# Optimization experiments

Hardware: AMD Instinct MI355X
Metric: run time of the kernel (lower is better)

Reference implementation:

```python
import jax, jax.numpy as jnp
import numpy as np

B, T, D, H = 8, 128, 768, 768  # batch, num tokens (actual==virtual), dim, hidden_dim
LN_EPS = 1e-5


def setup_inputs() -> dict:
    key = jax.random.key(0)
    ks = jax.random.split(key, 7)
    s1 = 1.0 / np.sqrt(D)  # torch nn.Linear init scale (uniform bound)
    s2 = 1.0 / np.sqrt(H)
    return {
        "x": jax.random.normal(ks[0], (B, T, D), dtype=jnp.float32),
        "gamma": jnp.ones((T, D), dtype=jnp.float32),
        "beta": jnp.zeros((T, D), dtype=jnp.float32),
        "W1": jax.random.uniform(ks[1], (T, D, H), minval=-s1, maxval=s1, dtype=jnp.float32),
        "b1": jax.random.uniform(ks[2], (T, H), minval=-s1, maxval=s1, dtype=jnp.float32),
        "W2": jax.random.uniform(ks[3], (T, H, D), minval=-s2, maxval=s2, dtype=jnp.float32),
        "b2": jax.random.uniform(ks[4], (T, D), minval=-s2, maxval=s2, dtype=jnp.float32),
    }


def reference(x, gamma, beta, W1, b1, W2, b2):
    # Per-token FeedForward with distinct weights per token position, fully batched
    # (equivalent to the per-token Python loop in the torch module, with
    # num_actual_tokens == num_virtual_tokens so no repeat happens).
    mu = jnp.mean(x, axis=-1, keepdims=True)
    var = jnp.mean(jnp.square(x - mu), axis=-1, keepdims=True)
    xn = (x - mu) * jax.lax.rsqrt(var + LN_EPS)
    xn = xn * gamma[None] + beta[None]                      # [B,T,D]
    h = jnp.einsum('btd,tdh->bth', xn, W1) + b1[None]       # [B,T,H]
    h = jax.nn.gelu(h, approximate=False)                   # torch nn.GELU default (erf)
    out = jnp.einsum('bth,thd->btd', h, W2) + b2[None]      # [B,T,D]
    return out + x  # residual
```

## Files before the change

### kernel.cpp

```cpp
#include <hip/hip_runtime.h>
#include <math.h>

#define TB 8
#define TT 128
#define TD 768
#define TH 768
#define LN_EPS 1e-5f

__global__ __launch_bounds__(256) void ln_kernel(
    const float* __restrict__ x,
    const float* __restrict__ gamma,
    const float* __restrict__ beta,
    float* __restrict__ xn) {
  const int w = threadIdx.x >> 6, lane = threadIdx.x & 63;
  const int r = blockIdx.x * 4 + w;
  const int t = r & (TT - 1);
  const int b = r >> 7;
  const float* xr = x + (size_t)r * TD;

  float v[12];
  float s = 0.f, ss = 0.f;
#pragma unroll
  for (int i = 0; i < 3; ++i) {
    float4 f = *(const float4*)(xr + i * 256 + lane * 4);
    v[i * 4 + 0] = f.x; v[i * 4 + 1] = f.y;
    v[i * 4 + 2] = f.z; v[i * 4 + 3] = f.w;
    s += f.x + f.y + f.z + f.w;
    ss += f.x * f.x + f.y * f.y + f.z * f.z + f.w * f.w;
  }
#pragma unroll
  for (int off = 32; off; off >>= 1) {
    s  += __shfl_down(s, off, 64);
    ss += __shfl_down(ss, off, 64);
  }
  s = __shfl(s, 0, 64); ss = __shfl(ss, 0, 64);
  const float mu   = s * (1.f / TD);
  const float var  = ss * (1.f / TD) - mu * mu;
  const float rstd = rsqrtf(var + LN_EPS);

#pragma unroll
  for (int i = 0; i < 3; ++i) {
    const int d = i * 256 + lane * 4;
    float4 g  = *(const float4*)(gamma + (size_t)t * TD + d);
    float4 be = *(const float4*)(beta  + (size_t)t * TD + d);
    float* o = xn + ((size_t)t * TD + d) * TB + b;
    o[0 * TB] = (v[i * 4 + 0] - mu) * rstd * g.x + be.x;
    o[1 * TB] = (v[i * 4 + 1] - mu) * rstd * g.y + be.y;
    o[2 * TB] = (v[i * 4 + 2] - mu) * rstd * g.z + be.z;
    o[3 * TB] = (v[i * 4 + 3] - mu) * rstd * g.w + be.w;
  }
}

__global__ __launch_bounds__(256) void ff1_kernel(
    const float* __restrict__ xn,
    const float* __restrict__ W1,
    const float* __restrict__ b1,
    float* __restrict__ hbuf) {
  __shared__ float st[TD * TB];
  __shared__ float red[4][8][128];
  const int tid = threadIdx.x;
  const int w = tid >> 6, lane = tid & 63;
  const int t = blockIdx.x / 6, slice = blockIdx.x % 6;

  {
    const float4* src = (const float4*)(xn + (size_t)t * TD * TB);
    float4* dst = (float4*)st;
#pragma unroll
    for (int i = 0; i < 6; ++i) dst[tid + i * 256] = src[tid + i * 256];
  }
  __syncthreads();

  const int half = lane >> 5;
  const int cg = (lane & 31) * 4;
  const int c = slice * 128 + cg;
  const int r0 = w * 192 + half * 96;
  const float* wp = W1 + ((size_t)t * TD + r0) * TH + c;
  const float* xb = st + r0 * TB;

  float acc[8][4];
#pragma unroll
  for (int b = 0; b < 8; ++b)
#pragma unroll
    for (int j = 0; j < 4; ++j) acc[b][j] = 0.f;

#pragma unroll 4
  for (int d = 0; d < 96; ++d) {
    const float4 wv = *(const float4*)wp;
    wp += TH;
    const float4 xa = *(const float4*)(xb + d * 8);
    const float4 xc = *(const float4*)(xb + d * 8 + 4);
    const float xv[8] = {xa.x, xa.y, xa.z, xa.w, xc.x, xc.y, xc.z, xc.w};
#pragma unroll
    for (int b = 0; b < 8; ++b) {
      acc[b][0] = fmaf(xv[b], wv.x, acc[b][0]);
      acc[b][1] = fmaf(xv[b], wv.y, acc[b][1]);
      acc[b][2] = fmaf(xv[b], wv.z, acc[b][2]);
      acc[b][3] = fmaf(xv[b], wv.w, acc[b][3]);
    }
  }

#pragma unroll
  for (int b = 0; b < 8; ++b)
#pragma unroll
    for (int j = 0; j < 4; ++j)
      acc[b][j] += __shfl_xor(acc[b][j], 32, 64);

  if (lane < 32) {
#pragma unroll
    for (int b = 0; b < 8; ++b)
      *(float4*)&red[w][b][cg] =
          make_float4(acc[b][0], acc[b][1], acc[b][2], acc[b][3]);
  }
  __syncthreads();

  {
    const int col = tid >> 1;
    const int bq = (tid & 1) * 4;
    const int cc = slice * 128 + col;
    const float bias = b1[(size_t)t * TH + cc];
    float4 o;
    float* po = (float*)&o;
#pragma unroll
    for (int i = 0; i < 4; ++i) {
      float v = red[0][bq + i][col] + red[1][bq + i][col] +
                red[2][bq + i][col] + red[3][bq + i][col] + bias;
      po[i] = 0.5f * v * (1.f + erff(v * 0.7071067811865476f));
    }
    *(float4*)(hbuf + ((size_t)t * TH + cc) * TB + bq) = o;
  }
}

__global__ __launch_bounds__(256) void ff2_kernel(
    const float* __restrict__ hbuf,
    const float* __restrict__ W2,
    const float* __restrict__ b2,
    const float* __restrict__ x,
    float* __restrict__ out) {
  __shared__ float st[TH * TB];
  __shared__ float red[4][8][128];
  const int tid = threadIdx.x;
  const int w = tid >> 6, lane = tid & 63;
  const int t = blockIdx.x / 6, slice = blockIdx.x % 6;

  {
    const float4* src = (const float4*)(hbuf + (size_t)t * TH * TB);
    float4* dst = (float4*)st;
#pragma unroll
    for (int i = 0; i < 6; ++i) dst[tid + i * 256] = src[tid + i * 256];
  }
  __syncthreads();

  const int half = lane >> 5;
  const int cg = (lane & 31) * 4;
  const int c = slice * 128 + cg;
  const int r0 = w * 192 + half * 96;
  const float* wp = W2 + ((size_t)t * TH + r0) * TD + c;
  const float* hb = st + r0 * TB;

  float acc[8][4];
#pragma unroll
  for (int b = 0; b < 8; ++b)
#pragma unroll
    for (int j = 0; j < 4; ++j) acc[b][j] = 0.f;

#pragma unroll 4
  for (int d = 0; d < 96; ++d) {
    const float4 wv = *(const float4*)wp;
    wp += TD;
    const float4 ha = *(const float4*)(hb + d * 8);
    const float4 hc = *(const float4*)(hb + d * 8 + 4);
    const float hv[8] = {ha.x, ha.y, ha.z, ha.w, hc.x, hc.y, hc.z, hc.w};
#pragma unroll
    for (int b = 0; b < 8; ++b) {
      acc[b][0] = fmaf(hv[b], wv.x, acc[b][0]);
      acc[b][1] = fmaf(hv[b], wv.y, acc[b][1]);
      acc[b][2] = fmaf(hv[b], wv.z, acc[b][2]);
      acc[b][3] = fmaf(hv[b], wv.w, acc[b][3]);
    }
  }

#pragma unroll
  for (int b = 0; b < 8; ++b)
#pragma unroll
    for (int j = 0; j < 4; ++j)
      acc[b][j] += __shfl_xor(acc[b][j], 32, 64);

  if (lane < 32) {
#pragma unroll
    for (int b = 0; b < 8; ++b)
      *(float4*)&red[w][b][cg] =
          make_float4(acc[b][0], acc[b][1], acc[b][2], acc[b][3]);
  }
  __syncthreads();

  {
    const int col = tid >> 1;
    const int bq = (tid & 1) * 4;
    const int cc = slice * 128 + col;
    const float bias = b2[(size_t)t * TD + cc];
#pragma unroll
    for (int i = 0; i < 4; ++i) {
      const size_t off = ((size_t)(bq + i) * TT + t) * TD + cc;
      float v = red[0][bq + i][col] + red[1][bq + i][col] +
                red[2][bq + i][col] + red[3][bq + i][col] + bias + x[off];
      out[off] = v;
    }
  }
}

extern "C" void kernel_launch(void* const* d_in, const int* in_sizes, int n_in,
                              void* d_out, int out_size, void* d_ws, size_t ws_size,
                              hipStream_t stream) {
  const float* x     = (const float*)d_in[0];
  const float* gamma = (const float*)d_in[1];
  const float* beta  = (const float*)d_in[2];
  const float* W1    = (const float*)d_in[3];
  const float* b1    = (const float*)d_in[4];
  const float* W2    = (const float*)d_in[5];
  const float* b2    = (const float*)d_in[6];
  float* out = (float*)d_out;

  float* xn   = (float*)d_ws;
  float* hbuf = xn + (size_t)TT * TD * TB;

  ln_kernel<<<256, 256, 0, stream>>>(x, gamma, beta, xn);
  ff1_kernel<<<TT * 6, 256, 0, stream>>>(xn, W1, b1, hbuf);
  ff2_kernel<<<TT * 6, 256, 0, stream>>>(hbuf, W2, b2, x, out);
}
```

Baseline: 121.3 us.

## Fuse LayerNorm into first GEMM and switch activations to batch-major layout

Folds the LayerNorm kernel into ff1, so each block normalizes its token's 8 batch rows straight into shared memory. This removes one launch and the xn workspace round trip. Shared and intermediate buffers change from d-major interleaved to [batch][dim] layout, which gives vectorized float4 stores for hbuf and the output and coalesced residual reads. The inner loops now load 4 weight rows per step and float4 activations per batch. The catch is that LayerNorm is recomputed in all 6 slice blocks per token (6x redundant LN work and x reads), and the stride-768 shared reads may cause bank conflicts.

```diff
diff --git a/kernel.cpp b/kernel.cpp
--- a/kernel.cpp
+++ b/kernel.cpp
@@ -7,75 +7,58 @@
 #define TH 768
 #define LN_EPS 1e-5f
 
-__global__ __launch_bounds__(256) void ln_kernel(
+__global__ __launch_bounds__(256) void ff1_kernel(
     const float* __restrict__ x,
     const float* __restrict__ gamma,
     const float* __restrict__ beta,
-    float* __restrict__ xn) {
-  const int w = threadIdx.x >> 6, lane = threadIdx.x & 63;
-  const int r = blockIdx.x * 4 + w;
-  const int t = r & (TT - 1);
-  const int b = r >> 7;
-  const float* xr = x + (size_t)r * TD;
-
-  float v[12];
-  float s = 0.f, ss = 0.f;
-#pragma unroll
-  for (int i = 0; i < 3; ++i) {
-    float4 f = *(const float4*)(xr + i * 256 + lane * 4);
-    v[i * 4 + 0] = f.x; v[i * 4 + 1] = f.y;
-    v[i * 4 + 2] = f.z; v[i * 4 + 3] = f.w;
-    s += f.x + f.y + f.z + f.w;
-    ss += f.x * f.x + f.y * f.y + f.z * f.z + f.w * f.w;
-  }
-#pragma unroll
-  for (int off = 32; off; off >>= 1) {
-    s  += __shfl_down(s, off, 64);
-    ss += __shfl_down(ss, off, 64);
-  }
-  s = __shfl(s, 0, 64); ss = __shfl(ss, 0, 64);
-  const float mu   = s * (1.f / TD);
-  const float var  = ss * (1.f / TD) - mu * mu;
-  const float rstd = rsqrtf(var + LN_EPS);
-
-#pragma unroll
-  for (int i = 0; i < 3; ++i) {
-    const int d = i * 256 + lane * 4;
-    float4 g  = *(const float4*)(gamma + (size_t)t * TD + d);
-    float4 be = *(const float4*)(beta  + (size_t)t * TD + d);
-    float* o = xn + ((size_t)t * TD + d) * TB + b;
-    o[0 * TB] = (v[i * 4 + 0] - mu) * rstd * g.x + be.x;
-    o[1 * TB] = (v[i * 4 + 1] - mu) * rstd * g.y + be.y;
-    o[2 * TB] = (v[i * 4 + 2] - mu) * rstd * g.z + be.z;
-    o[3 * TB] = (v[i * 4 + 3] - mu) * rstd * g.w + be.w;
-  }
-}
-
-__global__ __launch_bounds__(256) void ff1_kernel(
-    const float* __restrict__ xn,
     const float* __restrict__ W1,
     const float* __restrict__ b1,
     float* __restrict__ hbuf) {
-  __shared__ float st[TD * TB];
+  __shared__ float st[TB][TD];
   __shared__ float red[4][8][128];
   const int tid = threadIdx.x;
   const int w = tid >> 6, lane = tid & 63;
+  const int half = lane >> 5, l32 = lane & 31;
   const int t = blockIdx.x / 6, slice = blockIdx.x % 6;
 
   {
-    const float4* src = (const float4*)(xn + (size_t)t * TD * TB);
-    float4* dst = (float4*)st;
-#pragma unroll
-    for (int i = 0; i < 6; ++i) dst[tid + i * 256] = src[tid + i * 256];
-  }
-  __syncthreads();
-
-  const int half = lane >> 5;
-  const int cg = (lane & 31) * 4;
+    const int b = w * 2 + half;
+    const float* xr = x + ((size_t)b * TT + t) * TD;
+    float4 v[6];
+    float s = 0.f, ss = 0.f;
+#pragma unroll
+    for (int i = 0; i < 6; ++i) {
+      v[i] = *(const float4*)(xr + i * 128 + l32 * 4);
+      s += v[i].x + v[i].y + v[i].z + v[i].w;
+      ss += v[i].x * v[i].x + v[i].y * v[i].y + v[i].z * v[i].z + v[i].w * v[i].w;
+    }
+#pragma unroll
+    for (int off = 16; off; off >>= 1) {
+      s  += __shfl_xor(s, off, 64);
+      ss += __shfl_xor(ss, off, 64);
+    }
+    const float mu   = s * (1.f / TD);
+    const float var  = ss * (1.f / TD) - mu * mu;
+    const float rstd = rsqrtf(var + LN_EPS);
+#pragma unroll
+    for (int i = 0; i < 6; ++i) {
+      const int d = i * 128 + l32 * 4;
+      const float4 g  = *(const float4*)(gamma + (size_t)t * TD + d);
+      const float4 be = *(const float4*)(beta  + (size_t)t * TD + d);
+      float4 o;
+      o.x = (v[i].x - mu) * rstd * g.x + be.x;
+      o.y = (v[i].y - mu) * rstd * g.y + be.y;
+      o.z = (v[i].z - mu) * rstd * g.z + be.z;
+      o.w = (v[i].w - mu) * rstd * g.w + be.w;
+      *(float4*)&st[b][d] = o;
+    }
+  }
+  __syncthreads();
+
+  const int cg = l32 * 4;
   const int c = slice * 128 + cg;
   const int r0 = w * 192 + half * 96;
   const float* wp = W1 + ((size_t)t * TD + r0) * TH + c;
-  const float* xb = st + r0 * TB;
 
   float acc[8][4];
 #pragma unroll
@@ -83,20 +66,25 @@
 #pragma unroll
     for (int j = 0; j < 4; ++j) acc[b][j] = 0.f;
 
-#pragma unroll 4
-  for (int d = 0; d < 96; ++d) {
-    const float4 wv = *(const float4*)wp;
-    wp += TH;
-    const float4 xa = *(const float4*)(xb + d * 8);
-    const float4 xc = *(const float4*)(xb + d * 8 + 4);
-    const float xv[8] = {xa.x, xa.y, xa.z, xa.w, xc.x, xc.y, xc.z, xc.w};
-#pragma unroll
-    for (int b = 0; b < 8; ++b) {
-      acc[b][0] = fmaf(xv[b], wv.x, acc[b][0]);
-      acc[b][1] = fmaf(xv[b], wv.y, acc[b][1]);
-      acc[b][2] = fmaf(xv[b], wv.z, acc[b][2]);
-      acc[b][3] = fmaf(xv[b], wv.w, acc[b][3]);
-    }
+#pragma unroll 2
+  for (int dd = 0; dd < 96; dd += 4) {
+    float4 wv[4];
+#pragma unroll
+    for (int k = 0; k < 4; ++k) wv[k] = *(const float4*)(wp + k * TH);
+    wp += 4 * TH;
+    float4 xq[8];
+#pragma unroll
+    for (int b = 0; b < 8; ++b) xq[b] = *(const float4*)&st[b][r0 + dd];
+#pragma unroll
+    for (int k = 0; k < 4; ++k)
+#pragma unroll
+      for (int b = 0; b < 8; ++b) {
+        const float xv = ((const float*)&xq[b])[k];
+        acc[b][0] = fmaf(xv, wv[k].x, acc[b][0]);
+        acc[b][1] = fmaf(xv, wv[k].y, acc[b][1]);
+        acc[b][2] = fmaf(xv, wv[k].z, acc[b][2]);
+        acc[b][3] = fmaf(xv, wv[k].w, acc[b][3]);
+      }
   }
 
 #pragma unroll
@@ -114,19 +102,20 @@
   __syncthreads();
 
   {
-    const int col = tid >> 1;
-    const int bq = (tid & 1) * 4;
-    const int cc = slice * 128 + col;
-    const float bias = b1[(size_t)t * TH + cc];
+    const int b = tid >> 5;
+    const int colq = (tid & 31) * 4;
+    const int cc = slice * 128 + colq;
+    const float4 bias = *(const float4*)(b1 + (size_t)t * TH + cc);
     float4 o;
     float* po = (float*)&o;
-#pragma unroll
-    for (int i = 0; i < 4; ++i) {
-      float v = red[0][bq + i][col] + red[1][bq + i][col] +
-                red[2][bq + i][col] + red[3][bq + i][col] + bias;
-      po[i] = 0.5f * v * (1.f + erff(v * 0.7071067811865476f));
-    }
-    *(float4*)(hbuf + ((size_t)t * TH + cc) * TB + bq) = o;
+    const float* pb = (const float*)&bias;
+#pragma unroll
+    for (int k = 0; k < 4; ++k) {
+      float vv = red[0][b][colq + k] + red[1][b][colq + k] +
+                 red[2][b][colq + k] + red[3][b][colq + k] + pb[k];
+      po[k] = 0.5f * vv * (1.f + erff(vv * 0.7071067811865476f));
+    }
+    *(float4*)(hbuf + ((size_t)t * TB + b) * TH + cc) = o;
   }
 }
 
@@ -136,26 +125,25 @@
     const float* __restrict__ b2,
     const float* __restrict__ x,
     float* __restrict__ out) {
-  __shared__ float st[TH * TB];
+  __shared__ float st[TB][TH];
   __shared__ float red[4][8][128];
   const int tid = threadIdx.x;
   const int w = tid >> 6, lane = tid & 63;
+  const int half = lane >> 5, l32 = lane & 31;
   const int t = blockIdx.x / 6, slice = blockIdx.x % 6;
 
   {
-    const float4* src = (const float4*)(hbuf + (size_t)t * TH * TB);
-    float4* dst = (float4*)st;
+    const float4* src = (const float4*)(hbuf + (size_t)t * TB * TH);
+    float4* dst = (float4*)&st[0][0];
 #pragma unroll
     for (int i = 0; i < 6; ++i) dst[tid + i * 256] = src[tid + i * 256];
   }
   __syncthreads();
 
-  const int half = lane >> 5;
-  const int cg = (lane & 31) * 4;
+  const int cg = l32 * 4;
   const int c = slice * 128 + cg;
   const int r0 = w * 192 + half * 96;
   const float* wp = W2 + ((size_t)t * TH + r0) * TD + c;
-  const float* hb = st + r0 * TB;
 
   float acc[8][4];
 #pragma unroll
@@ -163,20 +151,25 @@
 #pragma unroll
     for (int j = 0; j < 4; ++j) acc[b][j] = 0.f;
 
-#pragma unroll 4
-  for (int d = 0; d < 96; ++d) {
-    const float4 wv = *(const float4*)wp;
-    wp += TD;
-    const float4 ha = *(const float4*)(hb + d * 8);
-    const float4 hc = *(const float4*)(hb + d * 8 + 4);
-    const float hv[8] = {ha.x, ha.y, ha.z, ha.w, hc.x, hc.y, hc.z, hc.w};
-#pragma unroll
-    for (int b = 0; b < 8; ++b) {
-      acc[b][0] = fmaf(hv[b], wv.x, acc[b][0]);
-      acc[b][1] = fmaf(hv[b], wv.y, acc[b][1]);
-      acc[b][2] = fmaf(hv[b], wv.z, acc[b][2]);
-      acc[b][3] = fmaf(hv[b], wv.w, acc[b][3]);
-    }
+#pragma unroll 2
+  for (int dd = 0; dd < 96; dd += 4) {
+    float4 wv[4];
+#pragma unroll
+    for (int k = 0; k < 4; ++k) wv[k] = *(const float4*)(wp + k * TD);
+    wp += 4 * TD;
+    float4 hq[8];
+#pragma unroll
+    for (int b = 0; b < 8; ++b) hq[b] = *(const float4*)&st[b][r0 + dd];
+#pragma unroll
+    for (int k = 0; k < 4; ++k)
+#pragma unroll
+      for (int b = 0; b < 8; ++b) {
+        const float hv = ((const float*)&hq[b])[k];
+        acc[b][0] = fmaf(hv, wv[k].x, acc[b][0]);
+        acc[b][1] = fmaf(hv, wv[k].y, acc[b][1]);
+        acc[b][2] = fmaf(hv, wv[k].z, acc[b][2]);
+        acc[b][3] = fmaf(hv, wv[k].w, acc[b][3]);
+      }
   }
 
 #pragma unroll
@@ -194,17 +187,21 @@
   __syncthreads();
 
   {
-    const int col = tid >> 1;
-    const int bq = (tid & 1) * 4;
-    const int cc = slice * 128 + col;
-    const float bias = b2[(size_t)t * TD + cc];
-#pragma unroll
-    for (int i = 0; i < 4; ++i) {
-      const size_t off = ((size_t)(bq + i) * TT + t) * TD + cc;
-      float v = red[0][bq + i][col] + red[1][bq + i][col] +
-                red[2][bq + i][col] + red[3][bq + i][col] + bias + x[off];
-      out[off] = v;
-    }
+    const int b = tid >> 5;
+    const int colq = (tid & 31) * 4;
+    const int cc = slice * 128 + colq;
+    const size_t off = ((size_t)b * TT + t) * TD + cc;
+    const float4 bias = *(const float4*)(b2 + (size_t)t * TD + cc);
+    const float4 xres = *(const float4*)(x + off);
+    float4 o;
+    float* po = (float*)&o;
+    const float* pb = (const float*)&bias;
+    const float* px = (const float*)&xres;
+#pragma unroll
+    for (int k = 0; k < 4; ++k)
+      po[k] = red[0][b][colq + k] + red[1][b][colq + k] +
+              red[2][b][colq + k] + red[3][b][colq + k] + pb[k] + px[k];
+    *(float4*)(out + off) = o;
   }
 }
 
@@ -220,10 +217,8 @@
   const float* b2    = (const float*)d_in[6];
   float* out = (float*)d_out;
 
-  float* xn   = (float*)d_ws;
-  float* hbuf = xn + (size_t)TT * TD * TB;
-
-  ln_kernel<<<256, 256, 0, stream>>>(x, gamma, beta, xn);
-  ff1_kernel<<<TT * 6, 256, 0, stream>>>(xn, W1, b1, hbuf);
+  float* hbuf = (float*)d_ws;
+
+  ff1_kernel<<<TT * 6, 256, 0, stream>>>(x, gamma, beta, W1, b1, hbuf);
   ff2_kernel<<<TT * 6, 256, 0, stream>>>(hbuf, W2, b2, x, out);
 }
```

Result: faster. 115.6 us (-4.7%).
